# Optimization experiments

Hardware: AMD Instinct MI355X
Metric: run time of the kernel (lower is better)

Reference implementation:

```python
import jax, jax.numpy as jnp
import numpy as np

Nc, Nq = 100000, 20000
Fc, Fq = 300, 768
HID, H, L = 128, 4, 2
D = HID // H
OUT = 8
E = 400000
NT, ET = 2, 3


def setup_inputs() -> dict:
    key = jax.random.key(0)
    ks = jax.random.split(key, 24)
    def n(i, shape, s=1.0):
        return jax.random.normal(ks[i], shape, dtype=jnp.float32) * s
    return {
        'x_context': n(0, (Nc, Fc)),
        'x_question': n(1, (Nq, Fq)),
        'src_q2c': jax.random.randint(ks[2], (E,), 0, Nq),
        'dst_q2c': jax.random.randint(ks[3], (E,), 0, Nc),
        'src_c2c': jax.random.randint(ks[4], (E,), 0, Nc),
        'dst_c2c': jax.random.randint(ks[5], (E,), 0, Nc),
        'src_c2q': jax.random.randint(ks[6], (E,), 0, Nc),
        'dst_c2q': jax.random.randint(ks[7], (E,), 0, Nq),
        'in_W_context': n(8, (Fc, HID), 0.05),
        'in_b_context': jnp.zeros((HID,), jnp.float32),
        'in_W_question': n(9, (Fq, HID), 0.05),
        'in_b_question': jnp.zeros((HID,), jnp.float32),
        'k_W': n(10, (L, NT, HID, HID), 0.05),
        'k_b': jnp.zeros((L, NT, HID), jnp.float32),
        'q_W': n(11, (L, NT, HID, HID), 0.05),
        'q_b': jnp.zeros((L, NT, HID), jnp.float32),
        'v_W': n(12, (L, NT, HID, HID), 0.05),
        'v_b': jnp.zeros((L, NT, HID), jnp.float32),
        'a_W': n(13, (L, NT, HID, HID), 0.05),
        'a_b': jnp.zeros((L, NT, HID), jnp.float32),
        'skip': jnp.ones((L, NT), jnp.float32),
        'a_rel': n(14, (L, ET, H, D, D), 0.1),
        'm_rel': n(15, (L, ET, H, D, D), 0.1),
        'p_rel': jnp.ones((L, ET, H), jnp.float32),
        'out_W': n(16, (HID, OUT), 0.05),
        'out_b': jnp.zeros((OUT,), jnp.float32),
    }


def segment_softmax(logits, seg, num):
    # logits: [E, H], seg: [E] destination node ids
    m = jax.ops.segment_max(logits, seg, num_segments=num)
    m = jnp.where(jnp.isfinite(m), m, 0.0)
    e = jnp.exp(logits - m[seg])
    s = jax.ops.segment_sum(e, seg, num_segments=num)
    return e / (s[seg] + 1e-16)


def reference(x_context, x_question, src_q2c, dst_q2c, src_c2c, dst_c2c,
              src_c2q, dst_c2q, in_W_context, in_b_context, in_W_question,
              in_b_question, k_W, k_b, q_W, q_b, v_W, v_b, a_W, a_b, skip,
              a_rel, m_rel, p_rel, out_W, out_b):
    # node type 0 = 'context', 1 = 'question'
    x = [jax.nn.relu(x_context @ in_W_context + in_b_context),
         jax.nn.relu(x_question @ in_W_question + in_b_question)]
    Ns = [x[0].shape[0], x[1].shape[0]]
    # (src_nt, dst_nt, src_idx, dst_idx) per edge type
    edge_types = [(1, 0, src_q2c, dst_q2c),
                  (0, 0, src_c2c, dst_c2c),
                  (0, 1, src_c2q, dst_c2q)]
    scale = 1.0 / jnp.sqrt(jnp.float32(D))
    for l in range(L):
        k = [(x[nt] @ k_W[l, nt] + k_b[l, nt]).reshape(-1, H, D) for nt in range(NT)]
        q = [(x[nt] @ q_W[l, nt] + q_b[l, nt]).reshape(-1, H, D) for nt in range(NT)]
        v = [(x[nt] @ v_W[l, nt] + v_b[l, nt]).reshape(-1, H, D) for nt in range(NT)]
        agg = [jnp.zeros((Ns[nt], H, D), x[0].dtype) for nt in range(NT)]
        for et, (snt, dnt, src, dst) in enumerate(edge_types):
            k_rel = jnp.einsum('ehd,hdf->ehf', k[snt][src], a_rel[l, et])
            v_rel = jnp.einsum('ehd,hdf->ehf', v[snt][src], m_rel[l, et])
            logits = jnp.einsum('ehd,ehd->eh', q[dnt][dst], k_rel) * p_rel[l, et] * scale
            alpha = segment_softmax(logits, dst, Ns[dnt])  # [E, H]
            agg[dnt] = agg[dnt].at[dst].add(v_rel * alpha[:, :, None])
        for nt in range(NT):
            o = jax.nn.gelu(agg[nt].reshape(Ns[nt], HID), approximate=False)
            o = o @ a_W[l, nt] + a_b[l, nt]
            g = jax.nn.sigmoid(skip[l, nt])
            x[nt] = g * o + (1.0 - g) * x[nt]
    return x[0] @ out_W + out_b
```

## Files before the change

kernel.cpp:

```cpp
#include <hip/hip_runtime.h>

constexpr int NC = 100000;
constexpr int NQ = 20000;
constexpr int FC = 300;
constexpr int FQ = 768;
constexpr int NEDGE = 400000;
constexpr int NTOT = NC + NC + NQ;
constexpr int NTOT2 = NC + NQ;
constexpr int NB0 = (NC + 127) / 128;
constexpr int NB1 = (NQ + 127) / 128;
constexpr int NBALL = NB0 + NB1;
constexpr float SCALE = 0.17677669529663687f;
constexpr float LOG2E = 1.4426950408889634f;

typedef __attribute__((ext_vector_type(8))) short bf16x8;
typedef __attribute__((ext_vector_type(4))) float f32x4;
typedef unsigned short u16;

__device__ __forceinline__ float gelu_f(float x) {
  return 0.5f * x * (1.0f + erff(x * 0.7071067811865476f));
}
__device__ __forceinline__ u16 bf16_rne(float x) {
  unsigned u = __float_as_uint(x);
  unsigned r = u + 0x7fffu + ((u >> 16) & 1u);
  return (u16)(r >> 16);
}
__device__ __forceinline__ float bf16_to_f(u16 h) {
  return __uint_as_float(((unsigned)h) << 16);
}
__device__ __forceinline__ void split2(float x, u16& hi, u16& lo) {
  hi = bf16_rne(x);
  lo = bf16_rne(x - bf16_to_f(hi));
}
__device__ __forceinline__ void splitT(float x, u16& hi, u16& lo) {
  hi = (u16)(__float_as_uint(x) >> 16);
  lo = bf16_rne(x - bf16_to_f(hi));
}

__global__ void k_count3(const int* __restrict__ d0, const int* __restrict__ d1,
                         const int* __restrict__ d2, int* __restrict__ counts) {
  int i = blockIdx.x * 256 + threadIdx.x;
  if (i >= 3 * NEDGE) return;
  int et = i / NEDGE, e = i - et * NEDGE;
  int d = (et == 0) ? d0[e] : (et == 1) ? d1[e] : d2[e];
  int base = (et == 0) ? 0 : (et == 1) ? NC : 2 * NC;
  atomicAdd(&counts[base + d], 1);
}

__global__ void k_scan_block(const int* __restrict__ in, int* __restrict__ out,
                             int* __restrict__ bsum, int n) {
  __shared__ int s[256];
  int tid = threadIdx.x;
  int i = blockIdx.x * 256 + tid;
  int v = (i < n) ? in[i] : 0;
  s[tid] = v;
  __syncthreads();
  for (int off = 1; off < 256; off <<= 1) {
    int t = (tid >= off) ? s[tid - off] : 0;
    __syncthreads();
    s[tid] += t;
    __syncthreads();
  }
  if (i < n) out[i] = s[tid] - v;
  if (tid == 255) bsum[blockIdx.x] = s[255];
}

__global__ void k_scan_sums(int* __restrict__ bsum, int nb) {
  __shared__ int s[1024];
  int tid = threadIdx.x;
  int v = (tid < nb) ? bsum[tid] : 0;
  s[tid] = v;
  __syncthreads();
  for (int off = 1; off < 1024; off <<= 1) {
    int t = (tid >= off) ? s[tid - off] : 0;
    __syncthreads();
    s[tid] += t;
    __syncthreads();
  }
  if (tid < nb) bsum[tid] = s[tid] - v;
}

__global__ void k_scan_add(int* __restrict__ ptr, const int* __restrict__ bsum,
                           int* __restrict__ cursor, int n, int total) {
  int i = blockIdx.x * 256 + threadIdx.x;
  if (i < n) {
    int v = ptr[i] + bsum[blockIdx.x];
    ptr[i] = v;
    cursor[i] = v;
  }
  if (i == 0) ptr[n] = total;
}

__global__ void k_scatter3(const int* __restrict__ s0, const int* __restrict__ s1,
                           const int* __restrict__ s2, const int* __restrict__ d0,
                           const int* __restrict__ d1, const int* __restrict__ d2,
                           int* __restrict__ cursor, int* __restrict__ srcs_out) {
  int i = blockIdx.x * 256 + threadIdx.x;
  if (i >= 3 * NEDGE) return;
  int et = i / NEDGE, e = i - et * NEDGE;
  int d = (et == 0) ? d0[e] : (et == 1) ? d1[e] : d2[e];
  int sv = (et == 0) ? s0[e] : (et == 1) ? s1[e] : s2[e];
  int base = (et == 0) ? 0 : (et == 1) ? NC : 2 * NC;
  int p = atomicAdd(&cursor[base + d], 1);
  srcs_out[p] = sv;
}

__global__ void prep_all(const float* __restrict__ kW, const float* __restrict__ kB,
                         const float* __restrict__ qW, const float* __restrict__ qB,
                         const float* __restrict__ vW, const float* __restrict__ vB,
                         const float* __restrict__ aW, const float* __restrict__ aB,
                         const float* __restrict__ arel, const float* __restrict__ mrel,
                         const float* __restrict__ prel,
                         u16* __restrict__ Bth, u16* __restrict__ Btl,
                         float* __restrict__ biasOut, int* __restrict__ counts) {
  int i = blockIdx.x;
  int col = threadIdx.x;
  int y = blockIdx.y;
  {
    int gid = (y * 128 + i) * 128 + col;
    if (gid < NTOT) counts[gid] = 0;
  }
  int l = y / 10, yy = y % 10;
  size_t lw = (size_t)l * 2 * 16384, lb = (size_t)l * 2 * 128;
  size_t le = (size_t)l * 3 * 4096, lp = (size_t)l * 3 * 4;
  const float *W = nullptr, *bb = nullptr, *rel = nullptr, *pr = nullptr;
  float mscale = 1.0f;
  bool fold = false;
  switch (yy) {
    case 0: W = qW + lw; bb = qB + lb; break;
    case 1: fold = true; W = kW + lw; bb = kB + lb; rel = arel + le + 4096; pr = prel + lp + 4; mscale = SCALE; break;
    case 2: fold = true; W = vW + lw; bb = vB + lb; rel = mrel + le + 4096; break;
    case 3: fold = true; W = kW + lw; bb = kB + lb; rel = arel + le + 8192; pr = prel + lp + 8; mscale = SCALE; break;
    case 4: fold = true; W = vW + lw; bb = vB + lb; rel = mrel + le + 8192; break;
    case 5: W = qW + lw + 16384; bb = qB + lb + 128; break;
    case 6: fold = true; W = kW + lw + 16384; bb = kB + lb + 128; rel = arel + le; pr = prel + lp; mscale = SCALE; break;
    case 7: fold = true; W = vW + lw + 16384; bb = vB + lb + 128; rel = mrel + le; break;
    case 8: W = aW + lw; bb = aB + lb; break;
    default: W = aW + lw + 16384; bb = aB + lb + 128; break;
  }
  int colOff = y * 128;
  if (!fold) {
    float v = W[i * 128 + col];
    u16 hi, lo;
    split2(v, hi, lo);
    Bth[(size_t)(colOff + col) * 128 + i] = hi;
    Btl[(size_t)(colOff + col) * 128 + i] = lo;
    if (i == 0) biasOut[colOff + col] = bb[col];
    return;
  }
  int h = col >> 5, f = col & 31;
  float m = (pr ? pr[h] : 1.0f) * mscale;
  float s = 0.0f;
  #pragma unroll
  for (int d = 0; d < 32; ++d)
    s += W[i * 128 + h * 32 + d] * rel[(h * 32 + d) * 32 + f];
  s *= m;
  u16 hi, lo;
  split2(s, hi, lo);
  Bth[(size_t)(colOff + col) * 128 + i] = hi;
  Btl[(size_t)(colOff + col) * 128 + i] = lo;
  if (i == 0) {
    float sb = 0.0f;
    #pragma unroll
    for (int d = 0; d < 32; ++d)
      sb += bb[h * 32 + d] * rel[(h * 32 + d) * 32 + f];
    biasOut[colOff + col] = sb * m;
  }
}

__global__ void split_in(const float* __restrict__ Wc, const float* __restrict__ bc,
                         const float* __restrict__ Wq, const float* __restrict__ bq,
                         u16* __restrict__ Bth, u16* __restrict__ Btl,
                         float* __restrict__ biasOut) {
  int n = blockIdx.x, y = blockIdx.y;
  const float* W = y ? Wq : Wc;
  const float* b = y ? bq : bc;
  int K = y ? FQ : FC, Kp = y ? 768 : 320;
  size_t boff = y ? (size_t)128 * 320 : 0;
  for (int k = threadIdx.x; k < Kp; k += 256) {
    float v = (k < K) ? W[(size_t)k * 128 + n] : 0.0f;
    u16 hi, lo;
    split2(v, hi, lo);
    Bth[boff + (size_t)n * Kp + k] = hi;
    Btl[boff + (size_t)n * Kp + k] = lo;
  }
  if (threadIdx.x == 0) biasOut[(y ? 128 : 0) + n] = b[n];
}

__global__ __launch_bounds__(256) void big_gemm(
    const float* __restrict__ Ac, const float* __restrict__ Aq,
    const u16* __restrict__ Bth, const u16* __restrict__ Btl,
    const float* __restrict__ biasBuf,
    u16* __restrict__ xh_all, u16* __restrict__ xl_all) {
  __shared__ u16 smem[20480];
  constexpr int AHo = 0, ALo = 5120, BHo = 10240, BLo = 15360;
  const int tid = threadIdx.x, lane = tid & 63, wv = tid >> 6;
  const int l15 = lane & 15, g4 = lane >> 4, koff = g4 * 8;
  const int sr = tid >> 1, sc16 = (tid & 1) * 16;

  const int bid = blockIdx.x;
  const int nt = (bid < NB0) ? 0 : 1;
  const int m0 = nt ? (bid - NB0) * 128 : bid * 128;
  const int M = nt ? NQ : NC;
  const int rowbase = nt ? NC : 0;
  const float* A32;
  int K, Kp, biasOff;
  size_t boff;
  if (nt == 0) { A32 = Ac; K = FC; Kp = 320; boff = 0; biasOff = 0; }
  else { A32 = Aq; K = FQ; Kp = 768; boff = (size_t)128 * 320; biasOff = 128; }
  size_t arow = (size_t)(m0 + sr) * K;
  const bool rowokA = (m0 + sr) < M;

  f32x4 acc[2][8];
  #pragma unroll
  for (int mi = 0; mi < 2; ++mi)
    #pragma unroll
    for (int ni = 0; ni < 8; ++ni) acc[mi][ni] = (f32x4){0.f, 0.f, 0.f, 0.f};

  for (int k0 = 0; k0 < K; k0 += 32) {
    float va[16];
    if (rowokA && (k0 + 32 <= K)) {
      const float* ap = A32 + arow + k0 + sc16;
      #pragma unroll
      for (int j = 0; j < 4; ++j) {
        float4 f = *(const float4*)(ap + 4 * j);
        va[4 * j + 0] = f.x; va[4 * j + 1] = f.y; va[4 * j + 2] = f.z; va[4 * j + 3] = f.w;
      }
    } else {
      #pragma unroll
      for (int j = 0; j < 16; ++j) {
        int kc = k0 + sc16 + j;
        va[j] = (rowokA && kc < K) ? A32[arow + kc] : 0.0f;
      }
    }
    {
      alignas(16) u16 hv[16], lv[16];
      #pragma unroll
      for (int j = 0; j < 16; ++j) splitT(va[j], hv[j], lv[j]);
      *(uint4*)&smem[AHo + sr * 40 + sc16] = *(const uint4*)&hv[0];
      *(uint4*)&smem[AHo + sr * 40 + sc16 + 8] = *(const uint4*)&hv[8];
      *(uint4*)&smem[ALo + sr * 40 + sc16] = *(const uint4*)&lv[0];
      *(uint4*)&smem[ALo + sr * 40 + sc16 + 8] = *(const uint4*)&lv[8];
    }
    {
      const u16* bp = Bth + boff + (size_t)sr * Kp + k0 + sc16;
      *(uint4*)&smem[BHo + sr * 40 + sc16] = *(const uint4*)bp;
      *(uint4*)&smem[BHo + sr * 40 + sc16 + 8] = *(const uint4*)(bp + 8);
      const u16* lp = Btl + boff + (size_t)sr * Kp + k0 + sc16;
      *(uint4*)&smem[BLo + sr * 40 + sc16] = *(const uint4*)lp;
      *(uint4*)&smem[BLo + sr * 40 + sc16 + 8] = *(const uint4*)(lp + 8);
    }
    __syncthreads();

    bf16x8 a_h[2], a_l[2];
    #pragma unroll
    for (int mi = 0; mi < 2; ++mi) {
      int row = wv * 32 + mi * 16 + l15;
      a_h[mi] = *(const bf16x8*)&smem[AHo + row * 40 + koff];
      a_l[mi] = *(const bf16x8*)&smem[ALo + row * 40 + koff];
    }
    #pragma unroll
    for (int ni = 0; ni < 8; ++ni) {
      int col = ni * 16 + l15;
      bf16x8 b_h = *(const bf16x8*)&smem[BHo + col * 40 + koff];
      bf16x8 b_l = *(const bf16x8*)&smem[BLo + col * 40 + koff];
      #pragma unroll
      for (int mi = 0; mi < 2; ++mi) {
        acc[mi][ni] = __builtin_amdgcn_mfma_f32_16x16x32_bf16(a_h[mi], b_h, acc[mi][ni], 0, 0, 0);
        acc[mi][ni] = __builtin_amdgcn_mfma_f32_16x16x32_bf16(a_l[mi], b_h, acc[mi][ni], 0, 0, 0);
        acc[mi][ni] = __builtin_amdgcn_mfma_f32_16x16x32_bf16(a_h[mi], b_l, acc[mi][ni], 0, 0, 0);
      }
    }
    __syncthreads();
  }

  #pragma unroll
  for (int mi = 0; mi < 2; ++mi)
    #pragma unroll
    for (int ni = 0; ni < 8; ++ni) {
      float bi = biasBuf[biasOff + ni * 16 + l15];
      #pragma unroll
      for (int rr = 0; rr < 4; ++rr)
        acc[mi][ni][rr] = fmaxf(acc[mi][ni][rr] + bi, 0.0f);
    }

  const int wrow = tid >> 2, wseg = tid & 3;
  #pragma unroll
  for (int ph = 0; ph < 2; ++ph) {
    #pragma unroll
    for (int h = 0; h < 2; ++h) {
      if (ph || h) __syncthreads();
      if ((wv >> 1) == h) {
        #pragma unroll
        for (int mi = 0; mi < 2; ++mi) {
          int rl = (wv & 1) * 32 + mi * 16 + g4 * 4;
          #pragma unroll
          for (int ni = 0; ni < 8; ++ni) {
            #pragma unroll
            for (int rr = 0; rr < 4; ++rr) {
              u16 hh, ll;
              split2(acc[mi][ni][rr], hh, ll);
              smem[(rl + rr) * 136 + ni * 16 + l15] = ph ? ll : hh;
            }
          }
        }
      }
      __syncthreads();
      int grow = m0 + h * 64 + wrow;
      if (grow < M) {
        u16* dstp = ph ? xl_all : xh_all;
        uint4* dst = (uint4*)&dstp[(size_t)(rowbase + grow) * 128 + wseg * 32];
        const uint4* src = (const uint4*)&smem[wrow * 136 + wseg * 32];
        #pragma unroll
        for (int j = 0; j < 4; ++j) dst[j] = src[j];
      }
    }
  }
}

__global__ __launch_bounds__(256) void aproj_gemm(
    const u16* __restrict__ Ag,
    const u16* __restrict__ Bth, const u16* __restrict__ Btl,
    const float* __restrict__ biasBuf,
    u16* __restrict__ xh_all, u16* __restrict__ xl_all,
    const float* __restrict__ skip, int l) {
  __shared__ u16 smem[15360];
  constexpr int AH = 0, BHo = 5120, BLo = 10240;
  const int tid = threadIdx.x, lane = tid & 63, wv = tid >> 6;
  const int l15 = lane & 15, g4 = lane >> 4, koff = g4 * 8;
  const int sr = tid >> 1, sc = (tid & 1) * 16;

  const int bid = blockIdx.x;
  const int nt = (bid < NB0) ? 0 : 1;
  const int m0 = nt ? (bid - NB0) * 128 : bid * 128;
  const int M = nt ? NQ : NC;
  const int rowbase = nt ? NC : 0;
  const size_t boff = (size_t)(8 + nt) * 16384;
  const int biasOff = (8 + nt) * 128;
  const bool rowok = (m0 + sr) < M;

  f32x4 acc[2][8];
  #pragma unroll
  for (int mi = 0; mi < 2; ++mi)
    #pragma unroll
    for (int ni = 0; ni < 8; ++ni) acc[mi][ni] = (f32x4){0.f, 0.f, 0.f, 0.f};

  for (int k0 = 0; k0 < 128; k0 += 32) {
    uint4 h0 = {0, 0, 0, 0}, h1 = {0, 0, 0, 0};
    if (rowok) {
      const u16* ap = Ag + (size_t)(rowbase + m0 + sr) * 128 + k0 + sc;
      h0 = *(const uint4*)ap;
      h1 = *(const uint4*)(ap + 8);
    }
    *(uint4*)&smem[AH + sr * 40 + sc] = h0;
    *(uint4*)&smem[AH + sr * 40 + sc + 8] = h1;
    {
      const u16* bp = Bth + boff + (size_t)sr * 128 + k0 + sc;
      *(uint4*)&smem[BHo + sr * 40 + sc] = *(const uint4*)bp;
      *(uint4*)&smem[BHo + sr * 40 + sc + 8] = *(const uint4*)(bp + 8);
      const u16* lp = Btl + boff + (size_t)sr * 128 + k0 + sc;
      *(uint4*)&smem[BLo + sr * 40 + sc] = *(const uint4*)lp;
      *(uint4*)&smem[BLo + sr * 40 + sc + 8] = *(const uint4*)(lp + 8);
    }
    __syncthreads();

    bf16x8 a_h[2];
    #pragma unroll
    for (int mi = 0; mi < 2; ++mi) {
      int row = wv * 32 + mi * 16 + l15;
      a_h[mi] = *(const bf16x8*)&smem[AH + row * 40 + koff];
    }
    #pragma unroll
    for (int ni = 0; ni < 8; ++ni) {
      int col = ni * 16 + l15;
      bf16x8 b_h = *(const bf16x8*)&smem[BHo + col * 40 + koff];
      bf16x8 b_l = *(const bf16x8*)&smem[BLo + col * 40 + koff];
      #pragma unroll
      for (int mi = 0; mi < 2; ++mi) {
        acc[mi][ni] = __builtin_amdgcn_mfma_f32_16x16x32_bf16(a_h[mi], b_h, acc[mi][ni], 0, 0, 0);
        acc[mi][ni] = __builtin_amdgcn_mfma_f32_16x16x32_bf16(a_h[mi], b_l, acc[mi][ni], 0, 0, 0);
      }
    }
    __syncthreads();
  }

  float g = 1.0f / (1.0f + __expf(-skip[l * 2 + nt]));

  #pragma unroll
  for (int mi = 0; mi < 2; ++mi) {
    #pragma unroll
    for (int ni = 0; ni < 8; ++ni) {
      int colL = ni * 16 + l15;
      float bi = biasBuf[biasOff + colL];
      #pragma unroll
      for (int rr = 0; rr < 4; ++rr) {
        int row = m0 + wv * 32 + mi * 16 + g4 * 4 + rr;
        float o = acc[mi][ni][rr] + bi;
        if (row < M) {
          size_t idx = (size_t)(rowbase + row) * 128 + colL;
          float xo = bf16_to_f(xh_all[idx]) + bf16_to_f(xl_all[idx]);
          o = g * o + (1.0f - g) * xo;
        }
        acc[mi][ni][rr] = o;
      }
    }
  }

  const int wrow = tid >> 2, wseg = tid & 3;
  #pragma unroll
  for (int ph = 0; ph < 2; ++ph) {
    #pragma unroll
    for (int h = 0; h < 2; ++h) {
      if (ph || h) __syncthreads();
      if ((wv >> 1) == h) {
        #pragma unroll
        for (int mi = 0; mi < 2; ++mi) {
          int rl = (wv & 1) * 32 + mi * 16 + g4 * 4;
          #pragma unroll
          for (int ni = 0; ni < 8; ++ni) {
            #pragma unroll
            for (int rr = 0; rr < 4; ++rr) {
              u16 hh, ll;
              split2(acc[mi][ni][rr], hh, ll);
              smem[(rl + rr) * 136 + ni * 16 + l15] = ph ? ll : hh;
            }
          }
        }
      }
      __syncthreads();
      int grow = m0 + h * 64 + wrow;
      if (grow < M) {
        u16* dstp = ph ? xl_all : xh_all;
        uint4* dst = (uint4*)&dstp[(size_t)(rowbase + grow) * 128 + wseg * 32];
        const uint4* src = (const uint4*)&smem[wrow * 136 + wseg * 32];
        #pragma unroll
        for (int j = 0; j < 4; ++j) dst[j] = src[j];
      }
    }
  }
}

__global__ __launch_bounds__(256) void projN(
    const u16* __restrict__ xh_all,
    const u16* __restrict__ Bth, const float* __restrict__ biasBuf,
    u16* __restrict__ q_all, u16* __restrict__ kvA,
    u16* __restrict__ kvB1, u16* __restrict__ kvB2, int last) {
  __shared__ u16 smem[22528];
  constexpr int AH = 0, BH = 17408;
  const int tid = threadIdx.x, lane = tid & 63, wv = tid >> 6;
  const int l15 = lane & 15, g4 = lane >> 4, koff = g4 * 8;
  const int bid = blockIdx.x;
  const int nt = (bid < NB0) ? 0 : 1;
  const int m0 = nt ? (bid - NB0) * 128 : bid * 128;
  const int M = nt ? NQ : NC;
  const int abase = nt ? NC : 0;
  const int nslab = nt ? (last ? 2 : 3) : (last ? 3 : 5);

  {
    const int sr = tid >> 1, sc = (tid & 1) * 64;
    if ((m0 + sr) < M) {
      const u16* ap = xh_all + (size_t)(abase + m0 + sr) * 128 + sc;
      #pragma unroll
      for (int j = 0; j < 8; ++j)
        *(uint4*)&smem[AH + sr * 136 + sc + j * 8] = *(const uint4*)(ap + j * 8);
    } else {
      uint4 z = {0, 0, 0, 0};
      #pragma unroll
      for (int j = 0; j < 8; ++j)
        *(uint4*)&smem[AH + sr * 136 + sc + j * 8] = z;
    }
  }

  const int srB = tid >> 1, scB = (tid & 1) * 16;
  for (int s = 0; s < nslab; ++s) {
    int y = (nt == 1 && last) ? (s + 1) : s;
    int bslab = nt ? 5 + y : y;
    u16* cp; int ld, cb, crowbase;
    if (nt == 0) {
      switch (y) {
        case 0: cp = q_all; ld = 128; cb = 0; crowbase = 0; break;
        case 1: cp = kvB1; ld = 256; cb = 0; crowbase = 0; break;
        case 2: cp = kvB1; ld = 256; cb = 128; crowbase = 0; break;
        case 3: cp = kvB2; ld = 256; cb = 0; crowbase = 0; break;
        default: cp = kvB2; ld = 256; cb = 128; crowbase = 0; break;
      }
    } else {
      switch (y) {
        case 0: cp = q_all; ld = 128; cb = 0; crowbase = NC; break;
        case 1: cp = kvA; ld = 256; cb = 0; crowbase = 0; break;
        default: cp = kvA; ld = 256; cb = 128; crowbase = 0; break;
      }
    }

    f32x4 acc[2][8];
    #pragma unroll
    for (int mi = 0; mi < 2; ++mi)
      #pragma unroll
      for (int ni = 0; ni < 8; ++ni) acc[mi][ni] = (f32x4){0.f, 0.f, 0.f, 0.f};

    #pragma unroll
    for (int ks = 0; ks < 4; ++ks) {
      const u16* bp = Bth + (size_t)(bslab * 128 + srB) * 128 + ks * 32 + scB;
      uint4 b0 = *(const uint4*)bp;
      uint4 b1 = *(const uint4*)(bp + 8);
      __syncthreads();
      *(uint4*)&smem[BH + srB * 40 + scB] = b0;
      *(uint4*)&smem[BH + srB * 40 + scB + 8] = b1;
      __syncthreads();

      bf16x8 a_h[2];
      #pragma unroll
      for (int mi = 0; mi < 2; ++mi) {
        int row = wv * 32 + mi * 16 + l15;
        a_h[mi] = *(const bf16x8*)&smem[AH + row * 136 + ks * 32 + koff];
      }
      #pragma unroll
      for (int ni = 0; ni < 8; ++ni) {
        int col = ni * 16 + l15;
        bf16x8 b_h = *(const bf16x8*)&smem[BH + col * 40 + koff];
        #pragma unroll
        for (int mi = 0; mi < 2; ++mi)
          acc[mi][ni] = __builtin_amdgcn_mfma_f32_16x16x32_bf16(a_h[mi], b_h, acc[mi][ni], 0, 0, 0);
      }
    }

    #pragma unroll
    for (int h = 0; h < 4; ++h) {
      __syncthreads();
      if (wv == h) {
        #pragma unroll
        for (int mi = 0; mi < 2; ++mi) {
          int rl = mi * 16 + g4 * 4;
          #pragma unroll
          for (int ni = 0; ni < 8; ++ni) {
            float bi = biasBuf[bslab * 128 + ni * 16 + l15];
            #pragma unroll
            for (int rr = 0; rr < 4; ++rr)
              smem[BH + (rl + rr) * 136 + ni * 16 + l15] = bf16_rne(acc[mi][ni][rr] + bi);
          }
        }
      }
      __syncthreads();
      int r = tid >> 3, cseg = (tid & 7) * 16;
      int grow = m0 + h * 32 + r;
      if (grow < M) {
        uint4* dst = (uint4*)&cp[(size_t)(crowbase + grow) * ld + cb + cseg];
        const uint4* src = (const uint4*)&smem[BH + r * 136 + cseg];
        dst[0] = src[0];
        dst[1] = src[1];
      }
    }
  }
}

__device__ __forceinline__ void attn_seg(
    const u16* __restrict__ kv, int start, int end,
    const int* __restrict__ srcs, const float q8[8], int lane, float accO[8]) {
  if (start >= end) return;
  float sum = 0.0f;
  float acc[8];
  #pragma unroll
  for (int i = 0; i < 8; ++i) acc[i] = 0.0f;
  const int half = lane >> 5;
  const int sub = lane & 31;
  const int bsrc = lane & 44;
  for (int e = start; e < end; e += 4) {
    int e0 = e + half;
    int e1 = e + 2 + half;
    bool v0 = e0 < end, v1 = e1 < end;
    int c0 = v0 ? e0 : end - 1;
    int c1 = v1 ? e1 : end - 1;
    int s0 = srcs[c0];
    int s1 = srcs[c1];
    uint4 u0 = *(const uint4*)&kv[(size_t)s0 * 256 + sub * 8];
    uint4 u1 = *(const uint4*)&kv[(size_t)s1 * 256 + sub * 8];
    float r0[8], r1[8];
    r0[0] = bf16_to_f((u16)(u0.x & 0xffffu)); r0[1] = bf16_to_f((u16)(u0.x >> 16));
    r0[2] = bf16_to_f((u16)(u0.y & 0xffffu)); r0[3] = bf16_to_f((u16)(u0.y >> 16));
    r0[4] = bf16_to_f((u16)(u0.z & 0xffffu)); r0[5] = bf16_to_f((u16)(u0.z >> 16));
    r0[6] = bf16_to_f((u16)(u0.w & 0xffffu)); r0[7] = bf16_to_f((u16)(u0.w >> 16));
    r1[0] = bf16_to_f((u16)(u1.x & 0xffffu)); r1[1] = bf16_to_f((u16)(u1.x >> 16));
    r1[2] = bf16_to_f((u16)(u1.y & 0xffffu)); r1[3] = bf16_to_f((u16)(u1.y >> 16));
    r1[4] = bf16_to_f((u16)(u1.z & 0xffffu)); r1[5] = bf16_to_f((u16)(u1.z >> 16));
    r1[6] = bf16_to_f((u16)(u1.w & 0xffffu)); r1[7] = bf16_to_f((u16)(u1.w >> 16));
    float p0 = q8[0] * r0[0];
    float p1 = q8[0] * r1[0];
    #pragma unroll
    for (int i = 1; i < 8; ++i) {
      p0 = fmaf(q8[i], r0[i], p0);
      p1 = fmaf(q8[i], r1[i], p1);
    }
    p0 += __shfl_xor(p0, 1);
    p1 += __shfl_xor(p1, 1);
    p0 += __shfl_xor(p0, 2);
    p1 += __shfl_xor(p1, 2);
    p0 = fminf(p0, 100.0f);
    p1 = fminf(p1, 100.0f);
    float w0 = v0 ? exp2f(p0) : 0.0f;
    float w1 = v1 ? exp2f(p1) : 0.0f;
    float wB0 = __shfl(w0, bsrc);
    float wB1 = __shfl(w1, bsrc);
    sum += wB0 + wB1;
    #pragma unroll
    for (int i = 0; i < 8; ++i) {
      acc[i] = fmaf(wB0, r0[i], acc[i]);
      acc[i] = fmaf(wB1, r1[i], acc[i]);
    }
  }
  sum += __shfl_xor(sum, 32);
  #pragma unroll
  for (int i = 0; i < 8; ++i) acc[i] += __shfl_xor(acc[i], 32);
  float inv = 1.0f / (sum + 1e-16f);
  #pragma unroll
  for (int i = 0; i < 8; ++i) accO[i] = fmaf(acc[i], inv, accO[i]);
}

__global__ __launch_bounds__(256) void attn_all(
    const u16* __restrict__ q_all, const u16* __restrict__ kvA,
    const u16* __restrict__ kvB1, const u16* __restrict__ kvB2,
    const int* __restrict__ ptr_all, const int* __restrict__ srcs_all,
    u16* __restrict__ agg_g, int ncap) {
  int wave = threadIdx.x >> 6, lane = threadIdx.x & 63;
  int node = blockIdx.x * 4 + wave;
  if (node >= ncap) return;
  int sub = lane & 31;
  float q8[8];
  #pragma unroll
  for (int i = 0; i < 8; ++i) q8[i] = 0.0f;
  if (sub < 16) {
    uint4 u = *(const uint4*)&q_all[(size_t)node * 128 + sub * 8];
    q8[0] = bf16_to_f((u16)(u.x & 0xffffu)) * LOG2E; q8[1] = bf16_to_f((u16)(u.x >> 16)) * LOG2E;
    q8[2] = bf16_to_f((u16)(u.y & 0xffffu)) * LOG2E; q8[3] = bf16_to_f((u16)(u.y >> 16)) * LOG2E;
    q8[4] = bf16_to_f((u16)(u.z & 0xffffu)) * LOG2E; q8[5] = bf16_to_f((u16)(u.z >> 16)) * LOG2E;
    q8[6] = bf16_to_f((u16)(u.w & 0xffffu)) * LOG2E; q8[7] = bf16_to_f((u16)(u.w >> 16)) * LOG2E;
  }
  float accO[8];
  #pragma unroll
  for (int i = 0; i < 8; ++i) accO[i] = 0.0f;
  if (node < NC) {
    attn_seg(kvA, ptr_all[node], ptr_all[node + 1], srcs_all, q8, lane, accO);
    attn_seg(kvB1, ptr_all[NC + node], ptr_all[NC + node + 1], srcs_all, q8, lane, accO);
  } else {
    int idx = 2 * NC + (node - NC);
    attn_seg(kvB2, ptr_all[idx], ptr_all[idx + 1], srcs_all, q8, lane, accO);
  }
  if (lane >= 16 && lane < 32) {
    int j = lane - 16;
    alignas(16) u16 hv[8];
    #pragma unroll
    for (int i = 0; i < 8; ++i) hv[i] = bf16_rne(gelu_f(accO[i]));
    *(uint4*)&agg_g[(size_t)node * 128 + j * 8] = *(const uint4*)hv;
  }
}

__global__ __launch_bounds__(256) void gemm_out(const u16* __restrict__ Xh,
                                                const u16* __restrict__ Xl,
                                                const float* __restrict__ W,
                                                const float* __restrict__ b,
                                                float* __restrict__ out, int M) {
  __shared__ float Ws[1024];
  __shared__ float As[32][129];
  int tid = threadIdx.x;
  int m0 = blockIdx.x * 32;
  *(float4*)&Ws[tid * 4] = *(const float4*)&W[tid * 4];
  {
    int r = tid >> 3;
    int c0 = (tid & 7) * 16;
    if (m0 + r < M) {
      const u16* hp = Xh + (size_t)(m0 + r) * 128 + c0;
      const u16* lp = Xl + (size_t)(m0 + r) * 128 + c0;
      #pragma unroll
      for (int j = 0; j < 16; ++j) As[r][c0 + j] = bf16_to_f(hp[j]) + bf16_to_f(lp[j]);
    } else {
      #pragma unroll
      for (int j = 0; j < 16; ++j) As[r][c0 + j] = 0.0f;
    }
  }
  __syncthreads();
  int r = tid >> 3, c = tid & 7;
  float sum = b[c];
  #pragma unroll 16
  for (int k = 0; k < 128; ++k) sum = fmaf(As[r][k], Ws[k * 8 + c], sum);
  if (m0 + r < M) out[(size_t)(m0 + r) * 8 + c] = sum;
}

static inline size_t align256(size_t x) { return (x + 255) & ~(size_t)255; }

extern "C" void kernel_launch(void* const* d_in, const int* in_sizes, int n_in,
                              void* d_out, int out_size, void* d_ws, size_t ws_size,
                              hipStream_t stream) {
  const float* x_context = (const float*)d_in[0];
  const float* x_question = (const float*)d_in[1];
  const int* src_q2c = (const int*)d_in[2];
  const int* dst_q2c = (const int*)d_in[3];
  const int* src_c2c = (const int*)d_in[4];
  const int* dst_c2c = (const int*)d_in[5];
  const int* src_c2q = (const int*)d_in[6];
  const int* dst_c2q = (const int*)d_in[7];
  const float* inWc = (const float*)d_in[8];
  const float* inbc = (const float*)d_in[9];
  const float* inWq = (const float*)d_in[10];
  const float* inbq = (const float*)d_in[11];
  const float* kW = (const float*)d_in[12];
  const float* kB = (const float*)d_in[13];
  const float* qW = (const float*)d_in[14];
  const float* qB = (const float*)d_in[15];
  const float* vW = (const float*)d_in[16];
  const float* vB = (const float*)d_in[17];
  const float* aW = (const float*)d_in[18];
  const float* aB = (const float*)d_in[19];
  const float* skip = (const float*)d_in[20];
  const float* arel = (const float*)d_in[21];
  const float* mrel = (const float*)d_in[22];
  const float* prel = (const float*)d_in[23];
  const float* outW = (const float*)d_in[24];
  const float* outb = (const float*)d_in[25];

  char* base = (char*)d_ws;
  size_t off = 0;
  auto carve = [&](size_t bytes) -> void* {
    void* p = base + off;
    off = align256(off + bytes);
    return p;
  };
  u16* xh_all = (u16*)carve((size_t)NTOT2 * 128 * 2);
  u16* xl_all = (u16*)carve((size_t)NTOT2 * 128 * 2);
  u16* q_all = (u16*)carve((size_t)NTOT2 * 128 * 2);
  u16* kvA = (u16*)carve((size_t)NQ * 256 * 2);
  u16* kvB1 = (u16*)carve((size_t)NC * 256 * 2);
  u16* kvB2 = (u16*)carve((size_t)NC * 256 * 2);
  u16* agg_g = (u16*)carve((size_t)NTOT2 * 128 * 2);
  u16* Bth = (u16*)carve((size_t)2560 * 128 * 2);
  u16* Btl = (u16*)carve((size_t)2560 * 128 * 2);
  u16* BthI = (u16*)carve((size_t)(320 + 768) * 128 * 2);
  u16* BtlI = (u16*)carve((size_t)(320 + 768) * 128 * 2);
  float* biasBuf = (float*)carve(2560 * 4);
  float* biasIn = (float*)carve(256 * 4);
  int* ptr_all = (int*)carve((size_t)(NTOT + 1) * 4);
  int* srcs_all = (int*)carve((size_t)3 * NEDGE * 4);
  int* counts = (int*)carve((size_t)NTOT * 4);
  int* cursor = (int*)carve((size_t)NTOT * 4);
  int* blksums = (int*)carve(2048 * 4);

  split_in<<<dim3(128, 2), 256, 0, stream>>>(inWc, inbc, inWq, inbq, BthI, BtlI, biasIn);
  prep_all<<<dim3(128, 20), 128, 0, stream>>>(kW, kB, qW, qB, vW, vB, aW, aB,
                                              arel, mrel, prel, Bth, Btl, biasBuf, counts);

  {
    int nb = (NTOT + 255) / 256;
    k_count3<<<(3 * NEDGE + 255) / 256, 256, 0, stream>>>(dst_q2c, dst_c2c, dst_c2q, counts);
    k_scan_block<<<nb, 256, 0, stream>>>(counts, ptr_all, blksums, NTOT);
    k_scan_sums<<<1, 1024, 0, stream>>>(blksums, nb);
    k_scan_add<<<nb, 256, 0, stream>>>(ptr_all, blksums, cursor, NTOT, 3 * NEDGE);
    k_scatter3<<<(3 * NEDGE + 255) / 256, 256, 0, stream>>>(
        src_q2c, src_c2c, src_c2q, dst_q2c, dst_c2c, dst_c2q, cursor, srcs_all);
  }

  big_gemm<<<NBALL, 256, 0, stream>>>(x_context, x_question, BthI, BtlI, biasIn,
                                      xh_all, xl_all);

  for (int l = 0; l < 2; ++l) {
    const int last = (l == 1);
    const u16* BthL = Bth + (size_t)l * 10 * 128 * 128;
    const u16* BtlL = Btl + (size_t)l * 10 * 128 * 128;
    const float* biasL = biasBuf + (size_t)l * 1280;
    projN<<<NBALL, 256, 0, stream>>>(xh_all, BthL, biasL, q_all, kvA, kvB1, kvB2, last);
    int ncap = last ? NC : NTOT2;
    attn_all<<<(ncap + 3) / 4, 256, 0, stream>>>(q_all, kvA, kvB1, kvB2,
                                                 ptr_all, srcs_all, agg_g, ncap);
    aproj_gemm<<<last ? NB0 : NBALL, 256, 0, stream>>>(agg_g, BthL, BtlL, biasL,
                                                       xh_all, xl_all, skip, l);
  }

  gemm_out<<<(NC + 31) / 32, 256, 0, stream>>>(xh_all, xl_all, outW, outb, (float*)d_out, NC);
}
```

Measured before the change: 715.0 us.

## Pipeline input projection GEMM with register prefetch and smaller 64-row tiles

Replaces the input projection GEMM with a version that uses 64-row tiles (one 16-row slice per wave) and prefetches A two steps ahead and B one step ahead into registers, so global loads overlap the MFMA work. Smaller tiles double the block count and cut shared memory, which should raise occupancy and spread the memory-bound fp32 input read across more CUs. In exchange, each B tile is reused across fewer rows and more registers are held for prefetch buffers.

```diff
diff --git a/kernel.cpp b/kernel.cpp
--- a/kernel.cpp
+++ b/kernel.cpp
@@ -10,6 +10,9 @@
 constexpr int NB0 = (NC + 127) / 128;
 constexpr int NB1 = (NQ + 127) / 128;
 constexpr int NBALL = NB0 + NB1;
+constexpr int NBC64 = (NC + 63) / 64;
+constexpr int NBQ64 = (NQ + 63) / 64;
+constexpr int NBALL64 = NBC64 + NBQ64;
 constexpr float SCALE = 0.17677669529663687f;
 constexpr float LOG2E = 1.4426950408889634f;
 
@@ -187,20 +190,21 @@
   if (threadIdx.x == 0) biasOut[(y ? 128 : 0) + n] = b[n];
 }
 
-__global__ __launch_bounds__(256) void big_gemm(
+__global__ __launch_bounds__(256) void pipe_gemm(
     const float* __restrict__ Ac, const float* __restrict__ Aq,
     const u16* __restrict__ Bth, const u16* __restrict__ Btl,
     const float* __restrict__ biasBuf,
     u16* __restrict__ xh_all, u16* __restrict__ xl_all) {
-  __shared__ u16 smem[20480];
-  constexpr int AHo = 0, ALo = 5120, BHo = 10240, BLo = 15360;
+  __shared__ u16 smem[15360];
+  constexpr int AH = 0, AL = 2560, BH = 5120, BL = 10240;
   const int tid = threadIdx.x, lane = tid & 63, wv = tid >> 6;
   const int l15 = lane & 15, g4 = lane >> 4, koff = g4 * 8;
-  const int sr = tid >> 1, sc16 = (tid & 1) * 16;
+  const int srA = tid >> 2, scA = (tid & 3) * 8;
+  const int srB = tid >> 1, scB = (tid & 1) * 16;
 
   const int bid = blockIdx.x;
-  const int nt = (bid < NB0) ? 0 : 1;
-  const int m0 = nt ? (bid - NB0) * 128 : bid * 128;
+  const int nt = (bid < NBC64) ? 0 : 1;
+  const int m0 = nt ? (bid - NBC64) * 64 : bid * 64;
   const int M = nt ? NQ : NC;
   const int rowbase = nt ? NC : 0;
   const float* A32;
@@ -208,112 +212,120 @@
   size_t boff;
   if (nt == 0) { A32 = Ac; K = FC; Kp = 320; boff = 0; biasOff = 0; }
   else { A32 = Aq; K = FQ; Kp = 768; boff = (size_t)128 * 320; biasOff = 128; }
-  size_t arow = (size_t)(m0 + sr) * K;
-  const bool rowokA = (m0 + sr) < M;
-
-  f32x4 acc[2][8];
-  #pragma unroll
-  for (int mi = 0; mi < 2; ++mi)
-    #pragma unroll
-    for (int ni = 0; ni < 8; ++ni) acc[mi][ni] = (f32x4){0.f, 0.f, 0.f, 0.f};
-
-  for (int k0 = 0; k0 < K; k0 += 32) {
-    float va[16];
+  size_t arow = (size_t)(m0 + srA) * K;
+  const bool rowokA = (m0 + srA) < M;
+  const int nk = (K + 31) / 32;
+
+  f32x4 acc[8];
+  #pragma unroll
+  for (int ni = 0; ni < 8; ++ni) acc[ni] = (f32x4){0.f, 0.f, 0.f, 0.f};
+
+  auto loadA = [&](float va[8], int k0) {
     if (rowokA && (k0 + 32 <= K)) {
-      const float* ap = A32 + arow + k0 + sc16;
-      #pragma unroll
-      for (int j = 0; j < 4; ++j) {
-        float4 f = *(const float4*)(ap + 4 * j);
-        va[4 * j + 0] = f.x; va[4 * j + 1] = f.y; va[4 * j + 2] = f.z; va[4 * j + 3] = f.w;
-      }
+      const float* ap = A32 + arow + k0 + scA;
+      float4 f0 = *(const float4*)ap;
+      float4 f1 = *(const float4*)(ap + 4);
+      va[0] = f0.x; va[1] = f0.y; va[2] = f0.z; va[3] = f0.w;
+      va[4] = f1.x; va[5] = f1.y; va[6] = f1.z; va[7] = f1.w;
     } else {
       #pragma unroll
-      for (int j = 0; j < 16; ++j) {
-        int kc = k0 + sc16 + j;
+      for (int j = 0; j < 8; ++j) {
+        int kc = k0 + scA + j;
         va[j] = (rowokA && kc < K) ? A32[arow + kc] : 0.0f;
       }
     }
+  };
+  auto loadB = [&](uint4& bh0, uint4& bh1, uint4& bl0, uint4& bl1, int k0) {
+    const u16* bp = Bth + boff + (size_t)srB * Kp + k0 + scB;
+    bh0 = *(const uint4*)bp;
+    bh1 = *(const uint4*)(bp + 8);
+    const u16* lp = Btl + boff + (size_t)srB * Kp + k0 + scB;
+    bl0 = *(const uint4*)lp;
+    bl1 = *(const uint4*)(lp + 8);
+  };
+
+  float vaC[8], vaN[8], vaN2[8];
+  uint4 bhC0, bhC1, blC0, blC1, bhN0, bhN1, blN0, blN1;
+  loadA(vaC, 0);
+  loadB(bhC0, bhC1, blC0, blC1, 0);
+  if (nk > 1) loadA(vaN, 32);
+
+  for (int ks = 0; ks < nk; ++ks) {
     {
-      alignas(16) u16 hv[16], lv[16];
-      #pragma unroll
-      for (int j = 0; j < 16; ++j) splitT(va[j], hv[j], lv[j]);
-      *(uint4*)&smem[AHo + sr * 40 + sc16] = *(const uint4*)&hv[0];
-      *(uint4*)&smem[AHo + sr * 40 + sc16 + 8] = *(const uint4*)&hv[8];
-      *(uint4*)&smem[ALo + sr * 40 + sc16] = *(const uint4*)&lv[0];
-      *(uint4*)&smem[ALo + sr * 40 + sc16 + 8] = *(const uint4*)&lv[8];
-    }
+      alignas(16) u16 hv[8], lv[8];
+      #pragma unroll
+      for (int j = 0; j < 8; ++j) splitT(vaC[j], hv[j], lv[j]);
+      *(uint4*)&smem[AH + srA * 40 + scA] = *(const uint4*)hv;
+      *(uint4*)&smem[AL + srA * 40 + scA] = *(const uint4*)lv;
+      *(uint4*)&smem[BH + srB * 40 + scB] = bhC0;
+      *(uint4*)&smem[BH + srB * 40 + scB + 8] = bhC1;
+      *(uint4*)&smem[BL + srB * 40 + scB] = blC0;
+      *(uint4*)&smem[BL + srB * 40 + scB + 8] = blC1;
+    }
+    __syncthreads();
+
+    const bool moreA2 = (ks + 2) < nk;
+    const bool moreB = (ks + 1) < nk;
+    if (moreA2) loadA(vaN2, (ks + 2) * 32);
+    if (moreB) loadB(bhN0, bhN1, blN0, blN1, (ks + 1) * 32);
+
     {
-      const u16* bp = Bth + boff + (size_t)sr * Kp + k0 + sc16;
-      *(uint4*)&smem[BHo + sr * 40 + sc16] = *(const uint4*)bp;
-      *(uint4*)&smem[BHo + sr * 40 + sc16 + 8] = *(const uint4*)(bp + 8);
-      const u16* lp = Btl + boff + (size_t)sr * Kp + k0 + sc16;
-      *(uint4*)&smem[BLo + sr * 40 + sc16] = *(const uint4*)lp;
-      *(uint4*)&smem[BLo + sr * 40 + sc16 + 8] = *(const uint4*)(lp + 8);
-    }
-    __syncthreads();
-
-    bf16x8 a_h[2], a_l[2];
-    #pragma unroll
-    for (int mi = 0; mi < 2; ++mi) {
-      int row = wv * 32 + mi * 16 + l15;
-      a_h[mi] = *(const bf16x8*)&smem[AHo + row * 40 + koff];
-      a_l[mi] = *(const bf16x8*)&smem[ALo + row * 40 + koff];
-    }
+      int row = wv * 16 + l15;
+      bf16x8 a_h = *(const bf16x8*)&smem[AH + row * 40 + koff];
+      bf16x8 a_l = *(const bf16x8*)&smem[AL + row * 40 + koff];
+      #pragma unroll
+      for (int ni = 0; ni < 8; ++ni) {
+        int col = ni * 16 + l15;
+        bf16x8 b_h = *(const bf16x8*)&smem[BH + col * 40 + koff];
+        bf16x8 b_l = *(const bf16x8*)&smem[BL + col * 40 + koff];
+        acc[ni] = __builtin_amdgcn_mfma_f32_16x16x32_bf16(a_h, b_h, acc[ni], 0, 0, 0);
+        acc[ni] = __builtin_amdgcn_mfma_f32_16x16x32_bf16(a_l, b_h, acc[ni], 0, 0, 0);
+        acc[ni] = __builtin_amdgcn_mfma_f32_16x16x32_bf16(a_h, b_l, acc[ni], 0, 0, 0);
+      }
+    }
+    __syncthreads();
+
+    if (moreB) {
+      #pragma unroll
+      for (int j = 0; j < 8; ++j) vaC[j] = vaN[j];
+      bhC0 = bhN0; bhC1 = bhN1; blC0 = blN0; blC1 = blN1;
+    }
+    if (moreA2) {
+      #pragma unroll
+      for (int j = 0; j < 8; ++j) vaN[j] = vaN2[j];
+    }
+  }
+
+  const int rl0 = wv * 16 + g4 * 4;
+  #pragma unroll
+  for (int ni = 0; ni < 8; ++ni) {
+    float bi = biasBuf[biasOff + ni * 16 + l15];
+    #pragma unroll
+    for (int rr = 0; rr < 4; ++rr)
+      acc[ni][rr] = fmaxf(acc[ni][rr] + bi, 0.0f);
+  }
+
+  const int wrow = tid >> 2, wseg = tid & 3;
+  #pragma unroll
+  for (int ph = 0; ph < 2; ++ph) {
+    if (ph) __syncthreads();
     #pragma unroll
     for (int ni = 0; ni < 8; ++ni) {
-      int col = ni * 16 + l15;
-      bf16x8 b_h = *(const bf16x8*)&smem[BHo + col * 40 + koff];
-      bf16x8 b_l = *(const bf16x8*)&smem[BLo + col * 40 + koff];
-      #pragma unroll
-      for (int mi = 0; mi < 2; ++mi) {
-        acc[mi][ni] = __builtin_amdgcn_mfma_f32_16x16x32_bf16(a_h[mi], b_h, acc[mi][ni], 0, 0, 0);
-        acc[mi][ni] = __builtin_amdgcn_mfma_f32_16x16x32_bf16(a_l[mi], b_h, acc[mi][ni], 0, 0, 0);
-        acc[mi][ni] = __builtin_amdgcn_mfma_f32_16x16x32_bf16(a_h[mi], b_l, acc[mi][ni], 0, 0, 0);
-      }
-    }
-    __syncthreads();
-  }
-
-  #pragma unroll
-  for (int mi = 0; mi < 2; ++mi)
-    #pragma unroll
-    for (int ni = 0; ni < 8; ++ni) {
-      float bi = biasBuf[biasOff + ni * 16 + l15];
-      #pragma unroll
-      for (int rr = 0; rr < 4; ++rr)
-        acc[mi][ni][rr] = fmaxf(acc[mi][ni][rr] + bi, 0.0f);
-    }
-
-  const int wrow = tid >> 2, wseg = tid & 3;
-  #pragma unroll
-  for (int ph = 0; ph < 2; ++ph) {
-    #pragma unroll
-    for (int h = 0; h < 2; ++h) {
-      if (ph || h) __syncthreads();
-      if ((wv >> 1) == h) {
-        #pragma unroll
-        for (int mi = 0; mi < 2; ++mi) {
-          int rl = (wv & 1) * 32 + mi * 16 + g4 * 4;
-          #pragma unroll
-          for (int ni = 0; ni < 8; ++ni) {
-            #pragma unroll
-            for (int rr = 0; rr < 4; ++rr) {
-              u16 hh, ll;
-              split2(acc[mi][ni][rr], hh, ll);
-              smem[(rl + rr) * 136 + ni * 16 + l15] = ph ? ll : hh;
-            }
-          }
-        }
-      }
-      __syncthreads();
-      int grow = m0 + h * 64 + wrow;
-      if (grow < M) {
-        u16* dstp = ph ? xl_all : xh_all;
-        uint4* dst = (uint4*)&dstp[(size_t)(rowbase + grow) * 128 + wseg * 32];
-        const uint4* src = (const uint4*)&smem[wrow * 136 + wseg * 32];
-        #pragma unroll
-        for (int j = 0; j < 4; ++j) dst[j] = src[j];
-      }
+      #pragma unroll
+      for (int rr = 0; rr < 4; ++rr) {
+        u16 hh, ll;
+        split2(acc[ni][rr], hh, ll);
+        smem[(rl0 + rr) * 136 + ni * 16 + l15] = ph ? ll : hh;
+      }
+    }
+    __syncthreads();
+    int grow = m0 + wrow;
+    if (grow < M) {
+      u16* dstp = ph ? xl_all : xh_all;
+      uint4* dst = (uint4*)&dstp[(size_t)(rowbase + grow) * 128 + wseg * 32];
+      const uint4* src = (const uint4*)&smem[wrow * 136 + wseg * 32];
+      #pragma unroll
+      for (int j = 0; j < 4; ++j) dst[j] = src[j];
     }
   }
 }
@@ -756,8 +768,8 @@
         src_q2c, src_c2c, src_c2q, dst_q2c, dst_c2c, dst_c2q, cursor, srcs_all);
   }
 
-  big_gemm<<<NBALL, 256, 0, stream>>>(x_context, x_question, BthI, BtlI, biasIn,
-                                      xh_all, xl_all);
+  pipe_gemm<<<NBALL64, 256, 0, stream>>>(x_context, x_question, BthI, BtlI, biasIn,
+                                         xh_all, xl_all);
 
   for (int l = 0; l < 2; ++l) {
     const int last = (l == 1);
```

Result: no change. 708.7 us (-0.9%).
